# Optimization experiments

Hardware: AMD Instinct MI355X
Metric: run time of the kernel (lower is better)

Reference implementation:

```python
import jax, jax.numpy as jnp
import numpy as np

N_GRAPHS = 2048
BN_EPS = 1e-5


def _lin_init(k, fan_in, fan_out):
    kw, kb = jax.random.split(k)
    s = 1.0 / np.sqrt(fan_in)
    w = jax.random.uniform(kw, (fan_in, fan_out), minval=-s, maxval=s, dtype=jnp.float32)
    b = jax.random.uniform(kb, (fan_out,), minval=-s, maxval=s, dtype=jnp.float32)
    return w, b


def setup_inputs() -> dict:
    key = jax.random.key(0)
    ks = jax.random.split(key, 16)
    N, E, F, H, C = 100000, 600000, 7, 128, 2
    inp = {}
    inp["x"] = jax.random.normal(ks[0], (N, F), dtype=jnp.float32)
    inp["edge_index"] = jax.random.randint(ks[1], (2, E), 0, N)
    inp["edge_attr"] = jax.random.normal(ks[2], (E,), dtype=jnp.float32)  # ignored by GINConv
    inp["batch"] = jnp.sort(jax.random.randint(ks[3], (N,), 0, N_GRAPHS))
    # GINConv inner MLPs: [in, H, H]
    inp["g1_w1"], inp["g1_b1"] = _lin_init(ks[4], F, H)
    inp["g1_w2"], inp["g1_b2"] = _lin_init(ks[5], H, H)
    inp["g2_w1"], inp["g2_b1"] = _lin_init(ks[6], H, H)
    inp["g2_w2"], inp["g2_b2"] = _lin_init(ks[7], H, H)
    inp["g3_w1"], inp["g3_b1"] = _lin_init(ks[8], H, H)
    inp["g3_w2"], inp["g3_b2"] = _lin_init(ks[9], H, H)
    # JumpingKnowledge('cat') projection: 3H -> H
    inp["jk_w"], inp["jk_b"] = _lin_init(ks[10], 3 * H, H)
    # classifier MLP [H, H, C] with batch_norm on hidden layer
    inp["c1_w"], inp["c1_b"] = _lin_init(ks[11], H, H)
    inp["bn_g"] = jnp.ones((H,), jnp.float32)
    inp["bn_b"] = jnp.zeros((H,), jnp.float32)
    inp["c2_w"], inp["c2_b"] = _lin_init(ks[12], H, C)
    return inp


def reference(x, edge_index, edge_attr, batch,
              g1_w1, g1_b1, g1_w2, g1_b2,
              g2_w1, g2_b1, g2_w2, g2_b2,
              g3_w1, g3_b1, g3_w2, g3_b2,
              jk_w, jk_b, c1_w, c1_b, bn_g, bn_b, c2_w, c2_b):
    src, dst = edge_index[0], edge_index[1]
    N = x.shape[0]

    def gin_conv(h, w1, b1, w2, b2):
        # sum aggregation of neighbor messages; eps=0 -> (1+eps)*x + aggr = x + aggr
        agg = jax.ops.segment_sum(h[src], dst, num_segments=N)
        z = h + agg
        return jax.nn.relu(z @ w1 + b1) @ w2 + b2  # inner MLP, plain last layer

    # BasicGNN applies act (ReLU) after each conv; dropout=eval (identity)
    h1 = jax.nn.relu(gin_conv(x, g1_w1, g1_b1, g1_w2, g1_b2))
    h2 = jax.nn.relu(gin_conv(h1, g2_w1, g2_b1, g2_w2, g2_b2))
    h3 = jax.nn.relu(gin_conv(h2, g3_w1, g3_b1, g3_w2, g3_b2))

    h = jnp.concatenate([h1, h2, h3], axis=-1) @ jk_w + jk_b  # jk='cat' + final lin
    g = jax.ops.segment_sum(h, batch, num_segments=N_GRAPHS)  # global_add_pool -> [G, H]

    z = g @ c1_w + c1_b
    mu = z.mean(axis=0)
    var = z.var(axis=0)
    z = (z - mu) * jax.lax.rsqrt(var + BN_EPS) * bn_g + bn_b  # batch_norm (batch stats)
    z = jax.nn.relu(z)
    return z @ c2_w + c2_b  # [G, num_classes]
```

## Files before the change

kernel.cpp:

```cpp
#include <hip/hip_runtime.h>

#define NGRAPH 2048

typedef __attribute__((ext_vector_type(8))) short bf16x8;
typedef __attribute__((ext_vector_type(4))) float f32x4;
typedef __attribute__((ext_vector_type(8))) _Float16 h16x8;
typedef __attribute__((ext_vector_type(4))) _Float16 h16x4;

__device__ inline unsigned short bf16_rne(float f) {
  union { float f; unsigned u; } c; c.f = f;
  unsigned u = c.u + 0x7fffu + ((c.u >> 16) & 1u);
  return (unsigned short)(u >> 16);
}
__device__ inline float bf16_to_f32(unsigned short h) {
  union { float f; unsigned u; } c; c.u = ((unsigned)h) << 16;
  return c.f;
}

__global__ __launch_bounds__(256) void scan_onepass(
    const int* __restrict__ deg, int* __restrict__ rowstart, int* __restrict__ cursor,
    unsigned* __restrict__ scanst, int N, int E, int nchunk)
{
  __shared__ int tmp[256];
  __shared__ int sh_chunk;
  __shared__ int sh_exc;
  int tid = threadIdx.x;
  if (tid == 0) sh_chunk = (int)atomicAdd(&scanst[nchunk], 1u);
  __syncthreads();
  int cb = sh_chunk;
  int i = cb * 256 + tid;
  int v = (i < N) ? deg[i] : 0;
  tmp[tid] = v;
  __syncthreads();
#pragma unroll
  for (int off = 1; off < 256; off <<= 1) {
    int t = (tid >= off) ? tmp[tid - off] : 0;
    __syncthreads();
    tmp[tid] += t;
    __syncthreads();
  }
  int aggregate = tmp[255];

  if (tid == 0) {
    const unsigned VMASK = (1u << 30) - 1u;
    if (cb == 0) {
      atomicExch(&scanst[0], (2u << 30) | (unsigned)aggregate);
      sh_exc = 0;
    } else {
      atomicExch(&scanst[cb], (1u << 30) | (unsigned)aggregate);
      int excv = 0;
      int j = cb - 1;
      while (j >= 0) {
        unsigned s;
        do { s = atomicAdd(&scanst[j], 0u); } while ((s >> 30) == 0u);
        excv += (int)(s & VMASK);
        if ((s >> 30) == 2u) break;
        --j;
      }
      sh_exc = excv;
      atomicExch(&scanst[cb], (2u << 30) | (unsigned)(excv + aggregate));
    }
  }
  __syncthreads();
  int exc = sh_exc;
  if (i < N) {
    int rs = exc + tmp[tid] - v;
    rowstart[i] = rs;
    cursor[i] = rs;
  }
  if (cb == nchunk - 1 && tid == 0) rowstart[N] = E;
}

__global__ __launch_bounds__(256) void fill_eidx(
    const int* __restrict__ src, const int* __restrict__ dst,
    int* __restrict__ cursor, int* __restrict__ eidx, int E)
{
  int e = blockIdx.x * 256 + threadIdx.x;
  if (e >= E) return;
  int d = dst[e];
  int pos = atomicAdd(&cursor[d], 1);
  eidx[pos] = src[e];
}

struct WPs {
  const float* w[5];
  unsigned short* hi[5];
  unsigned short* lo[5];
};
__global__ __launch_bounds__(256) void prep_hist(
    WPs p, const float* __restrict__ x, _Float16* __restrict__ x8h, int N,
    const int* __restrict__ dst, int* __restrict__ deg, int E,
    float4* __restrict__ zeroBase, int zeroCount)
{
  int g = blockIdx.x * 256 + threadIdx.x;
  if (g < E) {
    atomicAdd(&deg[dst[g]], 1);
    return;
  }
  int q = g - E;
  if (q < 5 * 16384) {
    int m = q >> 14;
    int j = q & 16383;
    int c = j >> 3, e = j & 7;
    int t = c >> 8, kc = (c >> 6) & 3, lane = c & 63;
    int n = t * 16 + (lane & 15);
    int k = kc * 32 + (lane >> 4) * 8 + e;
    float w = p.w[m][k * 128 + n];
    unsigned short h = bf16_rne(w);
    p.hi[m][j] = h;
    p.lo[m][j] = bf16_rne(w - bf16_to_f32(h));
    return;
  }
  q -= 5 * 16384;
  if (q < N * 8) {
    int v = q >> 3, j = q & 7;
    x8h[q] = (_Float16)((j < 7) ? x[(long)v * 7 + j] : 0.f);
    return;
  }
  q -= N * 8;
  if (q < zeroCount) zeroBase[q] = (float4){0.f, 0.f, 0.f, 0.f};
}

__device__ inline void mfma_pass(
    const _Float16* __restrict__ zbuf,
    const unsigned short* __restrict__ Whi, const unsigned short* __restrict__ Wlo,
    int rw, int m16, int quad, int lane, f32x4 acc[8])
{
  int r = rw + m16;
  const _Float16* zrow = &zbuf[r * 128];
#pragma unroll
  for (int kc = 0; kc < 4; ++kc) {
    int cidx = kc * 4 + quad;
    h16x8 zh = *(const h16x8*)&zrow[((cidx + r) & 15) * 8];
    bf16x8 ah, al;
#pragma unroll
    for (int j = 0; j < 8; ++j) {
      float f = (float)zh[j];
      unsigned short h = bf16_rne(f);
      ah[j] = (short)h;
      al[j] = (short)bf16_rne(f - bf16_to_f32(h));
    }
#pragma unroll
    for (int t = 0; t < 8; ++t) {
      long cb = ((t * 4 + kc) * 64 + lane) * 8;
      bf16x8 bh = *(const bf16x8*)&Whi[cb];
      bf16x8 bl = *(const bf16x8*)&Wlo[cb];
      acc[t] = __builtin_amdgcn_mfma_f32_16x16x32_bf16(ah, bh, acc[t], 0, 0, 0);
      acc[t] = __builtin_amdgcn_mfma_f32_16x16x32_bf16(ah, bl, acc[t], 0, 0, 0);
      acc[t] = __builtin_amdgcn_mfma_f32_16x16x32_bf16(al, bh, acc[t], 0, 0, 0);
    }
  }
}

__global__ __launch_bounds__(256, 8) void fused_gin(
    const _Float16* __restrict__ H, const int* __restrict__ rowstart,
    const int* __restrict__ eidx,
    const unsigned short* __restrict__ W1hi, const unsigned short* __restrict__ W1lo,
    const float* __restrict__ B1,
    const unsigned short* __restrict__ W2hi, const unsigned short* __restrict__ W2lo,
    const float* __restrict__ B2,
    _Float16* __restrict__ Out, int M)
{
  __shared__ _Float16 zbuf[64 * 128];
  int tid = threadIdx.x;
  int rbase = blockIdx.x * 64;

  {
    int sub = tid & 15;
    int ng = tid >> 4;
    const _Float16* Hc = H + sub * 8;
#pragma unroll
    for (int it = 0; it < 4; ++it) {
      int r = it * 16 + ng;
      int v = rbase + r;
      int vc = (v < M) ? v : (M - 1);
      h16x8 sv = *(const h16x8*)&Hc[(long)vc * 128];
      float a0[8], a1[8];
#pragma unroll
      for (int j = 0; j < 8; ++j) { a0[j] = (float)sv[j]; a1[j] = 0.f; }
      int e0 = rowstart[vc], e1 = rowstart[vc + 1];
      int e = e0;
      for (; e + 4 <= e1; e += 4) {
        int s0 = eidx[e], s1 = eidx[e + 1], s2 = eidx[e + 2], s3 = eidx[e + 3];
        h16x8 h0 = *(const h16x8*)&Hc[(long)s0 * 128];
        h16x8 h1 = *(const h16x8*)&Hc[(long)s1 * 128];
        h16x8 h2 = *(const h16x8*)&Hc[(long)s2 * 128];
        h16x8 h3 = *(const h16x8*)&Hc[(long)s3 * 128];
#pragma unroll
        for (int j = 0; j < 8; ++j) {
          a0[j] += (float)h0[j] + (float)h2[j];
          a1[j] += (float)h1[j] + (float)h3[j];
        }
      }
      for (; e + 2 <= e1; e += 2) {
        int s0 = eidx[e], s1 = eidx[e + 1];
        h16x8 h0 = *(const h16x8*)&Hc[(long)s0 * 128];
        h16x8 h1 = *(const h16x8*)&Hc[(long)s1 * 128];
#pragma unroll
        for (int j = 0; j < 8; ++j) {
          a0[j] += (float)h0[j];
          a1[j] += (float)h1[j];
        }
      }
      if (e < e1) {
        int s = eidx[e];
        h16x8 h = *(const h16x8*)&Hc[(long)s * 128];
#pragma unroll
        for (int j = 0; j < 8; ++j) a1[j] += (float)h[j];
      }
      h16x8 zo;
#pragma unroll
      for (int j = 0; j < 8; ++j) zo[j] = (_Float16)(a0[j] + a1[j]);
      *(h16x8*)&zbuf[r * 128 + ((sub + r) & 15) * 8] = zo;
    }
  }
  __syncthreads();

  int lane = tid & 63;
  int wv = tid >> 6;
  int m16 = lane & 15;
  int quad = lane >> 4;
  int rw = wv * 16;

  f32x4 acc[8];
#pragma unroll
  for (int t = 0; t < 8; ++t) acc[t] = (f32x4){0.f, 0.f, 0.f, 0.f};
  mfma_pass(zbuf, W1hi, W1lo, rw, m16, quad, lane, acc);

  float bias[8];
#pragma unroll
  for (int t = 0; t < 8; ++t) bias[t] = B1[t * 16 + m16];

  __syncthreads();
#pragma unroll
  for (int i = 0; i < 4; ++i) {
    int r = rw + quad * 4 + i;
#pragma unroll
    for (int t = 0; t < 8; ++t) {
      int col = t * 16 + m16;
      int cidx = col >> 3;
      zbuf[r * 128 + ((cidx + r) & 15) * 8 + (col & 7)] =
          (_Float16)fmaxf(acc[t][i] + bias[t], 0.f);
    }
  }
  __syncthreads();

#pragma unroll
  for (int t = 0; t < 8; ++t) acc[t] = (f32x4){0.f, 0.f, 0.f, 0.f};
  mfma_pass(zbuf, W2hi, W2lo, rw, m16, quad, lane, acc);

#pragma unroll
  for (int t = 0; t < 8; ++t) bias[t] = B2[t * 16 + m16];

#pragma unroll
  for (int i = 0; i < 4; ++i) {
    int r = rbase + rw + quad * 4 + i;
    if (r < M) {
#pragma unroll
      for (int t = 0; t < 8; ++t) {
        float o = fmaxf(acc[t][i] + bias[t], 0.f);
        Out[(long)r * 128 + t * 16 + m16] = (_Float16)o;
      }
    }
  }
}

__global__ __launch_bounds__(256, 8) void fused_l1(
    const _Float16* __restrict__ x8h, const int* __restrict__ rowstart,
    const int* __restrict__ eidx,
    const float* __restrict__ W1, const float* __restrict__ B1,
    const unsigned short* __restrict__ W2hi, const unsigned short* __restrict__ W2lo,
    const float* __restrict__ B2, _Float16* __restrict__ Out, int M)
{
  __shared__ _Float16 ybuf[64 * 128];
  __shared__ float z1s[64][8];
  int tid = threadIdx.x;
  int rbase = blockIdx.x * 64;

  {
    int node = tid >> 2, sub = tid & 3;
    int v = rbase + node;
    int vc = (v < M) ? v : (M - 1);
    float a[8];
    if (sub == 0) {
      h16x8 sv = *(const h16x8*)&x8h[(long)vc * 8];
#pragma unroll
      for (int j = 0; j < 8; ++j) a[j] = (float)sv[j];
    } else {
#pragma unroll
      for (int j = 0; j < 8; ++j) a[j] = 0.f;
    }
    int e0 = rowstart[vc], e1 = rowstart[vc + 1];
    int e = e0 + sub;
    for (; e + 4 < e1; e += 8) {
      int s0 = eidx[e], s1 = eidx[e + 4];
      h16x8 h0 = *(const h16x8*)&x8h[(long)s0 * 8];
      h16x8 h1 = *(const h16x8*)&x8h[(long)s1 * 8];
#pragma unroll
      for (int j = 0; j < 8; ++j) a[j] += (float)h0[j] + (float)h1[j];
    }
    if (e < e1) {
      int s = eidx[e];
      h16x8 h = *(const h16x8*)&x8h[(long)s * 8];
#pragma unroll
      for (int j = 0; j < 8; ++j) a[j] += (float)h[j];
    }
#pragma unroll
    for (int j = 0; j < 8; ++j) {
      a[j] += __shfl_xor(a[j], 1, 64);
      a[j] += __shfl_xor(a[j], 2, 64);
    }
    if (sub == 0) {
#pragma unroll
      for (int j = 0; j < 8; ++j) z1s[node][j] = a[j];
    }
  }
  __syncthreads();

  {
    int c = tid & 127;
    int cidx = c >> 3, celt = c & 7;
    int rh0 = (tid >> 7) * 32;
    float w1r[7];
#pragma unroll
    for (int k = 0; k < 7; ++k) w1r[k] = W1[k * 128 + c];
    float b1 = B1[c];
#pragma unroll 4
    for (int rr = 0; rr < 32; ++rr) {
      int r = rh0 + rr;
      const float* zp = z1s[r];
      float a = b1;
#pragma unroll
      for (int k = 0; k < 7; ++k) a += zp[k] * w1r[k];
      ybuf[r * 128 + ((cidx + r) & 15) * 8 + celt] = (_Float16)fmaxf(a, 0.f);
    }
  }
  __syncthreads();

  int lane = tid & 63;
  int wv = tid >> 6;
  int m16 = lane & 15;
  int quad = lane >> 4;
  int rw = wv * 16;

  f32x4 acc[8];
#pragma unroll
  for (int t = 0; t < 8; ++t) acc[t] = (f32x4){0.f, 0.f, 0.f, 0.f};
  mfma_pass(ybuf, W2hi, W2lo, rw, m16, quad, lane, acc);

  float bias[8];
#pragma unroll
  for (int t = 0; t < 8; ++t) bias[t] = B2[t * 16 + m16];

#pragma unroll
  for (int i = 0; i < 4; ++i) {
    int r = rbase + rw + quad * 4 + i;
    if (r < M) {
#pragma unroll
      for (int t = 0; t < 8; ++t) {
        float o = fmaxf(acc[t][i] + bias[t], 0.f);
        Out[(long)r * 128 + t * 16 + m16] = (_Float16)o;
      }
    }
  }
}

__global__ __launch_bounds__(256) void pool_all(
    const _Float16* __restrict__ H1, const _Float16* __restrict__ H2,
    const _Float16* __restrict__ H3, const int* __restrict__ batch,
    float* __restrict__ P, float* __restrict__ cnt, int Nn)
{
  long t = (long)blockIdx.x * 256 + threadIdx.x;
  int cg = (int)(t & 31);
  int chunk = (int)(t >> 5);
  int i0 = chunk * 16;
  if (i0 >= Nn) return;
  int c = cg * 4;
  float4 a1 = {0.f,0.f,0.f,0.f}, a2 = {0.f,0.f,0.f,0.f}, a3 = {0.f,0.f,0.f,0.f};
  int curb = -1;
  float runc = 0.f;
  for (int ii = 0; ii < 16; ++ii) {
    int i = i0 + ii;
    if (i >= Nn) break;
    int b = batch[i];
    if (b != curb) {
      if (curb >= 0) {
        float* p = &P[(long)curb * 384 + c];
        atomicAdd(p + 0, a1.x); atomicAdd(p + 1, a1.y);
        atomicAdd(p + 2, a1.z); atomicAdd(p + 3, a1.w);
        atomicAdd(p + 128, a2.x); atomicAdd(p + 129, a2.y);
        atomicAdd(p + 130, a2.z); atomicAdd(p + 131, a2.w);
        atomicAdd(p + 256, a3.x); atomicAdd(p + 257, a3.y);
        atomicAdd(p + 258, a3.z); atomicAdd(p + 259, a3.w);
        if (cg == 0) atomicAdd(&cnt[curb], runc);
      }
      a1 = (float4){0.f,0.f,0.f,0.f};
      a2 = (float4){0.f,0.f,0.f,0.f};
      a3 = (float4){0.f,0.f,0.f,0.f};
      runc = 0.f;
      curb = b;
    }
    h16x4 v1 = *(const h16x4*)&H1[(long)i * 128 + c];
    h16x4 v2 = *(const h16x4*)&H2[(long)i * 128 + c];
    h16x4 v3 = *(const h16x4*)&H3[(long)i * 128 + c];
    a1.x += (float)v1[0]; a1.y += (float)v1[1]; a1.z += (float)v1[2]; a1.w += (float)v1[3];
    a2.x += (float)v2[0]; a2.y += (float)v2[1]; a2.z += (float)v2[2]; a2.w += (float)v2[3];
    a3.x += (float)v3[0]; a3.y += (float)v3[1]; a3.z += (float)v3[2]; a3.w += (float)v3[3];
    runc += 1.f;
  }
  if (curb >= 0) {
    float* p = &P[(long)curb * 384 + c];
    atomicAdd(p + 0, a1.x); atomicAdd(p + 1, a1.y);
    atomicAdd(p + 2, a1.z); atomicAdd(p + 3, a1.w);
    atomicAdd(p + 128, a2.x); atomicAdd(p + 129, a2.y);
    atomicAdd(p + 130, a2.z); atomicAdd(p + 131, a2.w);
    atomicAdd(p + 256, a3.x); atomicAdd(p + 257, a3.y);
    atomicAdd(p + 258, a3.z); atomicAdd(p + 259, a3.w);
    if (cg == 0) atomicAdd(&cnt[curb], runc);
  }
}

__global__ __launch_bounds__(256) void jk_gemm(
    const float* __restrict__ P, const float* __restrict__ cnt,
    const float* __restrict__ W, const float* __restrict__ B,
    float* __restrict__ G)
{
  __shared__ float pl[768];
  int tid = threadIdx.x, blk = blockIdx.x;
  for (int o = tid; o < 768; o += 256) pl[o] = P[(long)blk * 768 + o];
  __syncthreads();
  int rr = tid >> 7;
  int col = tid & 127;
  int row = blk * 2 + rr;
  float acc = cnt[row] * B[col];
#pragma unroll 8
  for (int k = 0; k < 384; ++k)
    acc += pl[rr * 384 + k] * W[k * 128 + col];
  G[(long)row * 128 + col] = acc;
}

__global__ __launch_bounds__(256) void gemm_bn(
    const float* __restrict__ Z,
    const float* __restrict__ W, const float* __restrict__ B,
    float* __restrict__ Out, float* __restrict__ bnstat, int M)
{
  __shared__ float wlds[128 * 128];
  int tid = threadIdx.x;
  {
    const float4* Ws = (const float4*)W;
    float4* Wd = (float4*)wlds;
#pragma unroll
    for (int i = 0; i < 16; ++i) Wd[i * 256 + tid] = Ws[i * 256 + tid];
  }
  __syncthreads();

  int rg = tid >> 5;
  int c0 = (tid & 31) * 4;
  int rbase = blockIdx.x * 64 + rg * 8;

  float acc[8][4];
#pragma unroll
  for (int i = 0; i < 8; ++i)
#pragma unroll
    for (int j = 0; j < 4; ++j) acc[i][j] = 0.f;

#pragma unroll 2
  for (int kc = 0; kc < 128; kc += 4) {
    float zv[8][4];
#pragma unroll
    for (int i = 0; i < 8; ++i) {
      float4 z = *(const float4*)&Z[(long)(rbase + i) * 128 + kc];
      zv[i][0] = z.x; zv[i][1] = z.y; zv[i][2] = z.z; zv[i][3] = z.w;
    }
#pragma unroll
    for (int kk = 0; kk < 4; ++kk) {
      float4 w = *(const float4*)&wlds[(kc + kk) * 128 + c0];
#pragma unroll
      for (int i = 0; i < 8; ++i) {
        float z = zv[i][kk];
        acc[i][0] += z * w.x; acc[i][1] += z * w.y;
        acc[i][2] += z * w.z; acc[i][3] += z * w.w;
      }
    }
  }

  float4 b = *(const float4*)&B[c0];
  float s[4] = {0.f, 0.f, 0.f, 0.f};
  float s2[4] = {0.f, 0.f, 0.f, 0.f};
#pragma unroll
  for (int i = 0; i < 8; ++i) {
    float4 o;
    o.x = acc[i][0] + b.x; o.y = acc[i][1] + b.y;
    o.z = acc[i][2] + b.z; o.w = acc[i][3] + b.w;
    *(float4*)&Out[(long)(rbase + i) * 128 + c0] = o;
    s[0] += o.x; s[1] += o.y; s[2] += o.z; s[3] += o.w;
    s2[0] += o.x * o.x; s2[1] += o.y * o.y; s2[2] += o.z * o.z; s2[3] += o.w * o.w;
  }
#pragma unroll
  for (int j = 0; j < 4; ++j) {
    atomicAdd(&bnstat[c0 + j], s[j]);
    atomicAdd(&bnstat[128 + c0 + j], s2[j]);
  }
}

__global__ __launch_bounds__(256) void bn_final(
    const float* __restrict__ ZC, const float* __restrict__ bnstat,
    const float* __restrict__ gma, const float* __restrict__ bta,
    const float* __restrict__ W2, const float* __restrict__ B2, float* __restrict__ out)
{
  __shared__ float scl[128], shf[128];
  int tid = threadIdx.x;
  if (tid < 128) {
    float mu = bnstat[tid] * (1.f / NGRAPH);
    float var = bnstat[128 + tid] * (1.f / NGRAPH) - mu * mu;
    float rs = rsqrtf(var + 1e-5f);
    float sc = gma[tid] * rs;
    scl[tid] = sc;
    shf[tid] = bta[tid] - mu * sc;
  }
  __syncthreads();
  int g = blockIdx.x * 256 + tid;
  if (g >= NGRAPH) return;
  float a0 = B2[0], a1 = B2[1];
#pragma unroll 4
  for (int h = 0; h < 128; ++h) {
    float zn = ZC[(long)g * 128 + h] * scl[h] + shf[h];
    zn = fmaxf(zn, 0.f);
    a0 += zn * W2[2 * h];
    a1 += zn * W2[2 * h + 1];
  }
  out[2 * g] = a0;
  out[2 * g + 1] = a1;
}

extern "C" void kernel_launch(void* const* d_in, const int* in_sizes, int n_in,
                              void* d_out, int out_size, void* d_ws, size_t ws_size,
                              hipStream_t stream)
{
  const float* x    = (const float*)d_in[0];
  const int*   ei   = (const int*)d_in[1];
  const int*   batch = (const int*)d_in[3];
  const float* g1w1 = (const float*)d_in[4];  const float* g1b1 = (const float*)d_in[5];
  const float* g1w2 = (const float*)d_in[6];  const float* g1b2 = (const float*)d_in[7];
  const float* g2w1 = (const float*)d_in[8];  const float* g2b1 = (const float*)d_in[9];
  const float* g2w2 = (const float*)d_in[10]; const float* g2b2 = (const float*)d_in[11];
  const float* g3w1 = (const float*)d_in[12]; const float* g3b1 = (const float*)d_in[13];
  const float* g3w2 = (const float*)d_in[14]; const float* g3b2 = (const float*)d_in[15];
  const float* jkw  = (const float*)d_in[16]; const float* jkb  = (const float*)d_in[17];
  const float* c1w  = (const float*)d_in[18]; const float* c1b  = (const float*)d_in[19];
  const float* bng  = (const float*)d_in[20]; const float* bnb  = (const float*)d_in[21];
  const float* c2w  = (const float*)d_in[22]; const float* c2b  = (const float*)d_in[23];

  const int N = in_sizes[3];
  const int E = in_sizes[1] / 2;
  const int* src = ei;
  const int* dst = ei + E;

  char* w = (char*)d_ws;
  auto alloc = [&](size_t bytes) {
    char* p = w;
    w += (bytes + 255) & ~(size_t)255;
    return p;
  };
  _Float16* hA = (_Float16*)alloc((size_t)N * 128 * 2);
  _Float16* hB = (_Float16*)alloc((size_t)N * 128 * 2);
  _Float16* hC = (_Float16*)alloc((size_t)N * 128 * 2);
  _Float16* x8h = (_Float16*)alloc((size_t)N * 8 * 2);
  float* P       = (float*)alloc((size_t)NGRAPH * 384 * 4);
  float* cnt     = (float*)alloc((size_t)NGRAPH * 4);
  float* bnstat  = (float*)alloc(256 * 4);
  float* gbuf = (float*)alloc((size_t)NGRAPH * 128 * 4);
  float* zc   = (float*)alloc((size_t)NGRAPH * 128 * 4);
  int* deg      = (int*)alloc((size_t)N * 4);
  unsigned* scanst = (unsigned*)alloc((size_t)1024 * 4);
  int* cursor   = (int*)alloc((size_t)N * 4);
  int* rowstart = (int*)alloc((size_t)(N + 1) * 4);
  int* eidx     = (int*)alloc((size_t)E * 4);
  unsigned short* wtbuf = (unsigned short*)alloc((size_t)5 * 2 * 16384 * 2);

  unsigned short* WThi[5];
  unsigned short* WTlo[5];
  for (int m = 0; m < 5; ++m) {
    WThi[m] = wtbuf + (size_t)m * 2 * 16384;
    WTlo[m] = WThi[m] + 16384;
  }

  const int nchunk = (N + 255) / 256;
  const int eb = (E + 255) / 256;

  hipMemsetAsync(deg, 0, (size_t)((char*)(scanst + 1024) - (char*)deg), stream);

  {
    WPs p;
    p.w[0] = g1w2; p.w[1] = g2w1; p.w[2] = g2w2; p.w[3] = g3w1; p.w[4] = g3w2;
    for (int m = 0; m < 5; ++m) { p.hi[m] = WThi[m]; p.lo[m] = WTlo[m]; }
    int zeroCount = (NGRAPH * 384 + NGRAPH + 256) / 4;
    int total = E + 5 * 16384 + N * 8 + zeroCount;
    prep_hist<<<(total + 255) / 256, 256, 0, stream>>>(p, x, x8h, N, dst, deg, E,
                                                       (float4*)P, zeroCount);
  }

  scan_onepass<<<nchunk, 256, 0, stream>>>(deg, rowstart, cursor, scanst, N, E, nchunk);
  fill_eidx<<<eb, 256, 0, stream>>>(src, dst, cursor, eidx, E);

  const int fBlocks = (N + 63) / 64;
  const int poolBlocks = (((N + 15) / 16) * 32 + 255) / 256;

  fused_l1<<<fBlocks, 256, 0, stream>>>(x8h, rowstart, eidx, g1w1, g1b1,
      WThi[0], WTlo[0], g1b2, hC, N);
  fused_gin<<<fBlocks, 256, 0, stream>>>(hC, rowstart, eidx,
      WThi[1], WTlo[1], g2b1, WThi[2], WTlo[2], g2b2, hB, N);
  fused_gin<<<fBlocks, 256, 0, stream>>>(hB, rowstart, eidx,
      WThi[3], WTlo[3], g3b1, WThi[4], WTlo[4], g3b2, hA, N);

  pool_all<<<poolBlocks, 256, 0, stream>>>(hC, hB, hA, batch, P, cnt, N);

  jk_gemm<<<NGRAPH / 2, 256, 0, stream>>>(P, cnt, jkw, jkb, gbuf);
  gemm_bn<<<NGRAPH / 64, 256, 0, stream>>>(gbuf, c1w, c1b, zc, bnstat, NGRAPH);
  bn_final<<<(NGRAPH + 255) / 256, 256, 0, stream>>>(zc, bnstat, bng, bnb, c2w, c2b, (float*)d_out);
}
```

Measured before the change: 447.7 us.

## Replace atomic global pooling with per-graph segment-offset reduction

Graph segment start offsets are now computed from the sorted batch array inside the prep kernel. Pooling then runs one block per graph that sums its contiguous node range directly and writes P and cnt without atomics. This removes the float atomics and the zero-fill of the P buffer. In exchange, the pooling work per block varies with graph size, only 192 of 256 threads do useful work, and the result relies on batch being sorted.

```diff
diff --git a/kernel.cpp b/kernel.cpp
--- a/kernel.cpp
+++ b/kernel.cpp
@@ -5,7 +5,7 @@
 typedef __attribute__((ext_vector_type(8))) short bf16x8;
 typedef __attribute__((ext_vector_type(4))) float f32x4;
 typedef __attribute__((ext_vector_type(8))) _Float16 h16x8;
-typedef __attribute__((ext_vector_type(4))) _Float16 h16x4;
+typedef __attribute__((ext_vector_type(2))) _Float16 h16x2;
 
 __device__ inline unsigned short bf16_rne(float f) {
   union { float f; unsigned u; } c; c.f = f;
@@ -90,7 +90,8 @@
 __global__ __launch_bounds__(256) void prep_hist(
     WPs p, const float* __restrict__ x, _Float16* __restrict__ x8h, int N,
     const int* __restrict__ dst, int* __restrict__ deg, int E,
-    float4* __restrict__ zeroBase, int zeroCount)
+    const int* __restrict__ batch, int* __restrict__ gstart,
+    float* __restrict__ bnstat)
 {
   int g = blockIdx.x * 256 + threadIdx.x;
   if (g < E) {
@@ -118,7 +119,15 @@
     return;
   }
   q -= N * 8;
-  if (q < zeroCount) zeroBase[q] = (float4){0.f, 0.f, 0.f, 0.f};
+  if (q < 256) { bnstat[q] = 0.f; return; }
+  q -= 256;
+  if (q < N) {
+    int b = batch[q];
+    int bp = (q > 0) ? batch[q - 1] : -1;
+    for (int gg = bp + 1; gg <= b; ++gg) gstart[gg] = q;
+    if (q == N - 1)
+      for (int gg = b + 1; gg <= NGRAPH; ++gg) gstart[gg] = N;
+  }
 }
 
 __device__ inline void mfma_pass(
@@ -365,59 +374,33 @@
   }
 }
 
-__global__ __launch_bounds__(256) void pool_all(
+__global__ __launch_bounds__(256) void pool_direct(
     const _Float16* __restrict__ H1, const _Float16* __restrict__ H2,
-    const _Float16* __restrict__ H3, const int* __restrict__ batch,
-    float* __restrict__ P, float* __restrict__ cnt, int Nn)
-{
-  long t = (long)blockIdx.x * 256 + threadIdx.x;
-  int cg = (int)(t & 31);
-  int chunk = (int)(t >> 5);
-  int i0 = chunk * 16;
-  if (i0 >= Nn) return;
-  int c = cg * 4;
-  float4 a1 = {0.f,0.f,0.f,0.f}, a2 = {0.f,0.f,0.f,0.f}, a3 = {0.f,0.f,0.f,0.f};
-  int curb = -1;
-  float runc = 0.f;
-  for (int ii = 0; ii < 16; ++ii) {
-    int i = i0 + ii;
-    if (i >= Nn) break;
-    int b = batch[i];
-    if (b != curb) {
-      if (curb >= 0) {
-        float* p = &P[(long)curb * 384 + c];
-        atomicAdd(p + 0, a1.x); atomicAdd(p + 1, a1.y);
-        atomicAdd(p + 2, a1.z); atomicAdd(p + 3, a1.w);
-        atomicAdd(p + 128, a2.x); atomicAdd(p + 129, a2.y);
-        atomicAdd(p + 130, a2.z); atomicAdd(p + 131, a2.w);
-        atomicAdd(p + 256, a3.x); atomicAdd(p + 257, a3.y);
-        atomicAdd(p + 258, a3.z); atomicAdd(p + 259, a3.w);
-        if (cg == 0) atomicAdd(&cnt[curb], runc);
-      }
-      a1 = (float4){0.f,0.f,0.f,0.f};
-      a2 = (float4){0.f,0.f,0.f,0.f};
-      a3 = (float4){0.f,0.f,0.f,0.f};
-      runc = 0.f;
-      curb = b;
-    }
-    h16x4 v1 = *(const h16x4*)&H1[(long)i * 128 + c];
-    h16x4 v2 = *(const h16x4*)&H2[(long)i * 128 + c];
-    h16x4 v3 = *(const h16x4*)&H3[(long)i * 128 + c];
-    a1.x += (float)v1[0]; a1.y += (float)v1[1]; a1.z += (float)v1[2]; a1.w += (float)v1[3];
-    a2.x += (float)v2[0]; a2.y += (float)v2[1]; a2.z += (float)v2[2]; a2.w += (float)v2[3];
-    a3.x += (float)v3[0]; a3.y += (float)v3[1]; a3.z += (float)v3[2]; a3.w += (float)v3[3];
-    runc += 1.f;
-  }
-  if (curb >= 0) {
-    float* p = &P[(long)curb * 384 + c];
-    atomicAdd(p + 0, a1.x); atomicAdd(p + 1, a1.y);
-    atomicAdd(p + 2, a1.z); atomicAdd(p + 3, a1.w);
-    atomicAdd(p + 128, a2.x); atomicAdd(p + 129, a2.y);
-    atomicAdd(p + 130, a2.z); atomicAdd(p + 131, a2.w);
-    atomicAdd(p + 256, a3.x); atomicAdd(p + 257, a3.y);
-    atomicAdd(p + 258, a3.z); atomicAdd(p + 259, a3.w);
-    if (cg == 0) atomicAdd(&cnt[curb], runc);
-  }
+    const _Float16* __restrict__ H3, const int* __restrict__ gstart,
+    float* __restrict__ P, float* __restrict__ cnt)
+{
+  int g = blockIdx.x;
+  int s = gstart[g], e = gstart[g + 1];
+  int tid = threadIdx.x;
+  if (tid == 0) cnt[g] = (float)(e - s);
+  if (tid >= 192) return;
+  int cp = tid * 2;
+  const _Float16* A = (cp < 128) ? H1 : ((cp < 256) ? H2 : H3);
+  int c = cp & 127;
+  float ax = 0.f, ay = 0.f, bx = 0.f, by = 0.f;
+  int i = s;
+  for (; i + 2 <= e; i += 2) {
+    h16x2 v0 = *(const h16x2*)&A[(long)i * 128 + c];
+    h16x2 v1 = *(const h16x2*)&A[(long)(i + 1) * 128 + c];
+    ax += (float)v0[0]; ay += (float)v0[1];
+    bx += (float)v1[0]; by += (float)v1[1];
+  }
+  if (i < e) {
+    h16x2 v0 = *(const h16x2*)&A[(long)i * 128 + c];
+    ax += (float)v0[0]; ay += (float)v0[1];
+  }
+  float2 o = {ax + bx, ay + by};
+  *(float2*)&P[(long)g * 384 + cp] = o;
 }
 
 __global__ __launch_bounds__(256) void jk_gemm(
@@ -576,6 +559,7 @@
   int* cursor   = (int*)alloc((size_t)N * 4);
   int* rowstart = (int*)alloc((size_t)(N + 1) * 4);
   int* eidx     = (int*)alloc((size_t)E * 4);
+  int* gstart   = (int*)alloc((size_t)(NGRAPH + 1) * 4);
   unsigned short* wtbuf = (unsigned short*)alloc((size_t)5 * 2 * 16384 * 2);
 
   unsigned short* WThi[5];
@@ -594,17 +578,15 @@
     WPs p;
     p.w[0] = g1w2; p.w[1] = g2w1; p.w[2] = g2w2; p.w[3] = g3w1; p.w[4] = g3w2;
     for (int m = 0; m < 5; ++m) { p.hi[m] = WThi[m]; p.lo[m] = WTlo[m]; }
-    int zeroCount = (NGRAPH * 384 + NGRAPH + 256) / 4;
-    int total = E + 5 * 16384 + N * 8 + zeroCount;
+    int total = E + 5 * 16384 + N * 8 + 256 + N;
     prep_hist<<<(total + 255) / 256, 256, 0, stream>>>(p, x, x8h, N, dst, deg, E,
-                                                       (float4*)P, zeroCount);
+                                                       batch, gstart, bnstat);
   }
 
   scan_onepass<<<nchunk, 256, 0, stream>>>(deg, rowstart, cursor, scanst, N, E, nchunk);
   fill_eidx<<<eb, 256, 0, stream>>>(src, dst, cursor, eidx, E);
 
   const int fBlocks = (N + 63) / 64;
-  const int poolBlocks = (((N + 15) / 16) * 32 + 255) / 256;
 
   fused_l1<<<fBlocks, 256, 0, stream>>>(x8h, rowstart, eidx, g1w1, g1b1,
       WThi[0], WTlo[0], g1b2, hC, N);
@@ -613,7 +595,7 @@
   fused_gin<<<fBlocks, 256, 0, stream>>>(hB, rowstart, eidx,
       WThi[3], WTlo[3], g3b1, WThi[4], WTlo[4], g3b2, hA, N);
 
-  pool_all<<<poolBlocks, 256, 0, stream>>>(hC, hB, hA, batch, P, cnt, N);
+  pool_direct<<<NGRAPH, 256, 0, stream>>>(hC, hB, hA, gstart, P, cnt);
 
   jk_gemm<<<NGRAPH / 2, 256, 0, stream>>>(P, cnt, jkw, jkb, gbuf);
   gemm_bn<<<NGRAPH / 64, 256, 0, stream>>>(gbuf, c1w, c1b, zc, bnstat, NGRAPH);
```

Result: faster. 410.4 us (-8.3%).
